# Kernel tuning notes

Measured on AMD Instinct MI355X. Metric: run time of the kernel, lower is better.

Reference implementation:

```python
import jax, jax.numpy as jnp
import numpy as np

N = 2_000_000  # number of Gaussians


def setup_inputs() -> dict:
    key = jax.random.key(0)
    k1, k2, k3 = jax.random.split(key, 3)
    quaternions = jax.random.normal(k1, (N, 4), dtype=jnp.float32)
    scales = jax.random.normal(k2, (N, 3), dtype=jnp.float32) * 0.5
    opacities = jax.random.normal(k3, (N, 1), dtype=jnp.float32)
    return {"quaternions": quaternions, "scales": scales, "opacities": opacities}


def quaternion_to_rotation_matrix(q):
    # q: [N,4] with layout (w, x, y, z) as in the torch source
    w, x, y, z = q[:, 0], q[:, 1], q[:, 2], q[:, 3]
    xx, yy, zz = x * x, y * y, z * z
    xy, xz, yz = x * y, x * z, y * z
    xw, yw, zw = x * w, y * w, z * w
    r0 = jnp.stack([1 - 2 * (yy + zz), 2 * (xy - zw), 2 * (xz + yw)], axis=-1)
    r1 = jnp.stack([2 * (xy + zw), 1 - 2 * (xx + zz), 2 * (yz - xw)], axis=-1)
    r2 = jnp.stack([2 * (xz - yw), 2 * (yz + xw), 1 - 2 * (xx + yy)], axis=-1)
    return jnp.stack([r0, r1, r2], axis=-2)  # [N,3,3]


def reference(quaternions, scales, opacities):
    # sigmoid applied to raw opacities (source: 1/(1+exp(-o)))
    opac = jax.nn.sigmoid(opacities)
    # NOTE: source normalizes by the GLOBAL Frobenius norm of the whole tensor
    # (to.linalg.norm with no dim) -- replicated faithfully.
    qn = quaternions / jnp.linalg.norm(quaternions)
    R = quaternion_to_rotation_matrix(qn)  # [N,3,3]
    # scales_d = (diag(exp(s)))**2 ; scales_i_d = (diag(1/exp(s)))**2
    s2 = jnp.exp(2.0 * scales)      # [N,3] diagonal of S^2
    inv_s2 = jnp.exp(-2.0 * scales)  # [N,3] diagonal of S^-2
    # cov = R @ diag(s2) @ R^T, inv_cov = R @ diag(inv_s2) @ R^T (closed form,
    # no batched 3x3 matmul chain / LAPACK inverse needed)
    cov = jnp.einsum('nij,nj,nkj->nik', R, s2, R)
    inv_cov = jnp.einsum('nij,nj,nkj->nik', R, inv_s2, R)
    return cov, inv_cov, opac
```

## Files before the change

kernel.cpp:

```cpp
#include <hip/hip_runtime.h>
#include <math.h>

#define RBLOCKS 1024
#define RTHREADS 256
#define CHUNK 256
#define BLOCK 256

typedef float f32x4 __attribute__((ext_vector_type(4)));

__global__ __launch_bounds__(RTHREADS) void gp_reduce_sq(
    const float4* __restrict__ q4, int n4, double* __restrict__ partials) {
    __shared__ double sdata[RTHREADS];
    double acc = 0.0;
    int stride = gridDim.x * blockDim.x;
    for (int i = blockIdx.x * blockDim.x + threadIdx.x; i < n4; i += stride) {
        float4 v = q4[i];
        acc += (double)v.x * v.x + (double)v.y * v.y +
               (double)v.z * v.z + (double)v.w * v.w;
    }
    sdata[threadIdx.x] = acc;
    __syncthreads();
    for (int s = RTHREADS / 2; s > 0; s >>= 1) {
        if (threadIdx.x < s) sdata[threadIdx.x] += sdata[threadIdx.x + s];
        __syncthreads();
    }
    if (threadIdx.x == 0) partials[blockIdx.x] = sdata[0];
}

__global__ __launch_bounds__(BLOCK) void gp_main(
    const float4* __restrict__ q,
    const float* __restrict__ scales,
    const float* __restrict__ opac_in,
    const double* __restrict__ partials,
    float* __restrict__ cov,
    float* __restrict__ inv_cov,
    float* __restrict__ opac_out,
    int n) {
    __shared__ union SU {
        double red[4];
        float mat[2 * CHUNK * 9];
    } u;
    __shared__ float s_sc[CHUNK * 3];

    const int tid = threadIdx.x;
    const int c0 = blockIdx.x * CHUNK;
    const int count = min(CHUNK, n - c0);

    float4 qi = make_float4(0.f, 0.f, 0.f, 0.f);
    float op = 0.f;
    if (tid < count) {
        qi = q[c0 + tid];
        op = opac_in[c0 + tid];
    }
    const int nsf = count * 3;
    const int nsf4 = nsf >> 2;
    const float4* sc4 = (const float4*)(scales + (size_t)c0 * 3);
    float4 sv = make_float4(0.f, 0.f, 0.f, 0.f);
    if (tid < nsf4) sv = sc4[tid];

    double acc = 0.0;
#pragma unroll
    for (int k = 0; k < RBLOCKS / 256; ++k) acc += partials[tid + 256 * k];
#pragma unroll
    for (int off = 32; off > 0; off >>= 1) acc += __shfl_down(acc, off);
    if ((tid & 63) == 0) u.red[tid >> 6] = acc;

    if (tid < nsf4) {
        s_sc[4 * tid + 0] = sv.x;
        s_sc[4 * tid + 1] = sv.y;
        s_sc[4 * tid + 2] = sv.z;
        s_sc[4 * tid + 3] = sv.w;
    }
    {
        int r = nsf - (nsf4 << 2);
        if (tid < r) s_sc[(nsf4 << 2) + tid] =
            scales[(size_t)c0 * 3 + (nsf4 << 2) + tid];
    }
    __syncthreads();

    double tot = u.red[0] + u.red[1] + u.red[2] + u.red[3];
    const float inv_norm = (float)(1.0 / sqrt(tot));
    __syncthreads();

    if (tid < count) {
        float w = qi.x * inv_norm;
        float x = qi.y * inv_norm;
        float y = qi.z * inv_norm;
        float z = qi.w * inv_norm;

        float xx = x * x, yy = y * y, zz = z * z;
        float xy = x * y, xz = x * z, yz = y * z;
        float xw = x * w, yw = y * w, zw = z * w;

        float r00 = 1.f - 2.f * (yy + zz);
        float r01 = 2.f * (xy - zw);
        float r02 = 2.f * (xz + yw);
        float r10 = 2.f * (xy + zw);
        float r11 = 1.f - 2.f * (xx + zz);
        float r12 = 2.f * (yz - xw);
        float r20 = 2.f * (xz - yw);
        float r21 = 2.f * (yz + xw);
        float r22 = 1.f - 2.f * (xx + yy);

        float s0 = s_sc[3 * tid + 0];
        float s1 = s_sc[3 * tid + 1];
        float s2 = s_sc[3 * tid + 2];

        float e0 = __expf(2.f * s0), e1 = __expf(2.f * s1), e2 = __expf(2.f * s2);
        float f0 = 1.f / e0, f1 = 1.f / e1, f2 = 1.f / e2;

        float* mc = &u.mat[tid * 9];
        float* mi = &u.mat[CHUNK * 9 + tid * 9];
        {
            float a0 = r00 * e0, a1 = r01 * e1, a2 = r02 * e2;
            float b0 = r10 * e0, b1 = r11 * e1, b2 = r12 * e2;
            float g0 = r20 * e0, g1 = r21 * e1, g2 = r22 * e2;
            float m00 = a0 * r00 + a1 * r01 + a2 * r02;
            float m01 = a0 * r10 + a1 * r11 + a2 * r12;
            float m02 = a0 * r20 + a1 * r21 + a2 * r22;
            float m11 = b0 * r10 + b1 * r11 + b2 * r12;
            float m12 = b0 * r20 + b1 * r21 + b2 * r22;
            float m22 = g0 * r20 + g1 * r21 + g2 * r22;
            mc[0] = m00; mc[1] = m01; mc[2] = m02;
            mc[3] = m01; mc[4] = m11; mc[5] = m12;
            mc[6] = m02; mc[7] = m12; mc[8] = m22;
        }
        {
            float a0 = r00 * f0, a1 = r01 * f1, a2 = r02 * f2;
            float b0 = r10 * f0, b1 = r11 * f1, b2 = r12 * f2;
            float g0 = r20 * f0, g1 = r21 * f1, g2 = r22 * f2;
            float m00 = a0 * r00 + a1 * r01 + a2 * r02;
            float m01 = a0 * r10 + a1 * r11 + a2 * r12;
            float m02 = a0 * r20 + a1 * r21 + a2 * r22;
            float m11 = b0 * r10 + b1 * r11 + b2 * r12;
            float m12 = b0 * r20 + b1 * r21 + b2 * r22;
            float m22 = g0 * r20 + g1 * r21 + g2 * r22;
            mi[0] = m00; mi[1] = m01; mi[2] = m02;
            mi[3] = m01; mi[4] = m11; mi[5] = m12;
            mi[6] = m02; mi[7] = m12; mi[8] = m22;
        }
        opac_out[c0 + tid] = 1.f / (1.f + __expf(-op));
    }
    __syncthreads();

    const int nf = count * 9;
    const int nfv = nf >> 2;
    f32x4* covo = (f32x4*)(cov + (size_t)c0 * 9);
    f32x4* invo = (f32x4*)(inv_cov + (size_t)c0 * 9);
    const f32x4* mc4 = (const f32x4*)u.mat;
    const f32x4* mi4 = (const f32x4*)(u.mat + CHUNK * 9);
    for (int j = tid; j < nfv; j += BLOCK) {
        __builtin_nontemporal_store(mc4[j], covo + j);
        __builtin_nontemporal_store(mi4[j], invo + j);
    }
    for (int j = (nfv << 2) + tid; j < nf; j += BLOCK) {
        cov[(size_t)c0 * 9 + j] = u.mat[j];
        inv_cov[(size_t)c0 * 9 + j] = u.mat[CHUNK * 9 + j];
    }
}

extern "C" void kernel_launch(void* const* d_in, const int* in_sizes, int n_in,
                              void* d_out, int out_size, void* d_ws, size_t ws_size,
                              hipStream_t stream) {
    const float4* q = (const float4*)d_in[0];
    const float* scales = (const float*)d_in[1];
    const float* opac = (const float*)d_in[2];
    int n = in_sizes[0] / 4;

    float* out = (float*)d_out;
    float* cov = out;
    float* inv_cov = out + (size_t)n * 9;
    float* opac_out = out + (size_t)n * 18;

    double* partials = (double*)d_ws;

    gp_reduce_sq<<<RBLOCKS, RTHREADS, 0, stream>>>(q, n, partials);

    int nblocks = (n + CHUNK - 1) / CHUNK;
    gp_main<<<nblocks, BLOCK, 0, stream>>>(
        q, scales, opac, partials, cov, inv_cov, opac_out, n);
}
```

Baseline: 43.61 us.

## Process two chunks per block in main kernel, amortizing partial reduction

Each block of the main kernel now handles two 256-element chunks instead of one, halving the grid. All global loads for both chunks are issued up front, and the reduction of the 1024 double partials to the global norm is done once for both. Chunk B's scales are staged into shared memory right after chunk A's stores are issued, and the opacity output now uses a nontemporal store. The cost is fewer blocks for latency hiding, more live registers, and an extra shared-memory reuse step with more barriers.

Result: slower. 45.23 us (+3.7%).

```diff
diff --git a/kernel.cpp b/kernel.cpp
--- a/kernel.cpp
+++ b/kernel.cpp
@@ -2,15 +2,14 @@
 #include <math.h>
 
 #define RBLOCKS 1024
-#define RTHREADS 256
+#define BLOCK 256
 #define CHUNK 256
-#define BLOCK 256
 
 typedef float f32x4 __attribute__((ext_vector_type(4)));
 
-__global__ __launch_bounds__(RTHREADS) void gp_reduce_sq(
+__global__ __launch_bounds__(BLOCK) void gp_reduce_sq(
     const float4* __restrict__ q4, int n4, double* __restrict__ partials) {
-    __shared__ double sdata[RTHREADS];
+    __shared__ double sdata[BLOCK];
     double acc = 0.0;
     int stride = gridDim.x * blockDim.x;
     for (int i = blockIdx.x * blockDim.x + threadIdx.x; i < n4; i += stride) {
@@ -20,11 +19,102 @@
     }
     sdata[threadIdx.x] = acc;
     __syncthreads();
-    for (int s = RTHREADS / 2; s > 0; s >>= 1) {
+    for (int s = BLOCK / 2; s > 0; s >>= 1) {
         if (threadIdx.x < s) sdata[threadIdx.x] += sdata[threadIdx.x + s];
         __syncthreads();
     }
     if (threadIdx.x == 0) partials[blockIdx.x] = sdata[0];
+}
+
+__device__ __forceinline__ void gp_compute_one(
+    int tid, float4 qi, float s0, float s1, float s2, float inv_norm,
+    float* __restrict__ s_mat) {
+    float w = qi.x * inv_norm;
+    float x = qi.y * inv_norm;
+    float y = qi.z * inv_norm;
+    float z = qi.w * inv_norm;
+
+    float xx = x * x, yy = y * y, zz = z * z;
+    float xy = x * y, xz = x * z, yz = y * z;
+    float xw = x * w, yw = y * w, zw = z * w;
+
+    float r00 = 1.f - 2.f * (yy + zz);
+    float r01 = 2.f * (xy - zw);
+    float r02 = 2.f * (xz + yw);
+    float r10 = 2.f * (xy + zw);
+    float r11 = 1.f - 2.f * (xx + zz);
+    float r12 = 2.f * (yz - xw);
+    float r20 = 2.f * (xz - yw);
+    float r21 = 2.f * (yz + xw);
+    float r22 = 1.f - 2.f * (xx + yy);
+
+    float e0 = __expf(2.f * s0), e1 = __expf(2.f * s1), e2 = __expf(2.f * s2);
+    float f0 = 1.f / e0, f1 = 1.f / e1, f2 = 1.f / e2;
+
+    float* mc = &s_mat[tid * 9];
+    float* mi = &s_mat[CHUNK * 9 + tid * 9];
+    {
+        float a0 = r00 * e0, a1 = r01 * e1, a2 = r02 * e2;
+        float b0 = r10 * e0, b1 = r11 * e1, b2 = r12 * e2;
+        float g0 = r20 * e0, g1 = r21 * e1, g2 = r22 * e2;
+        float m00 = a0 * r00 + a1 * r01 + a2 * r02;
+        float m01 = a0 * r10 + a1 * r11 + a2 * r12;
+        float m02 = a0 * r20 + a1 * r21 + a2 * r22;
+        float m11 = b0 * r10 + b1 * r11 + b2 * r12;
+        float m12 = b0 * r20 + b1 * r21 + b2 * r22;
+        float m22 = g0 * r20 + g1 * r21 + g2 * r22;
+        mc[0] = m00; mc[1] = m01; mc[2] = m02;
+        mc[3] = m01; mc[4] = m11; mc[5] = m12;
+        mc[6] = m02; mc[7] = m12; mc[8] = m22;
+    }
+    {
+        float a0 = r00 * f0, a1 = r01 * f1, a2 = r02 * f2;
+        float b0 = r10 * f0, b1 = r11 * f1, b2 = r12 * f2;
+        float g0 = r20 * f0, g1 = r21 * f1, g2 = r22 * f2;
+        float m00 = a0 * r00 + a1 * r01 + a2 * r02;
+        float m01 = a0 * r10 + a1 * r11 + a2 * r12;
+        float m02 = a0 * r20 + a1 * r21 + a2 * r22;
+        float m11 = b0 * r10 + b1 * r11 + b2 * r12;
+        float m12 = b0 * r20 + b1 * r21 + b2 * r22;
+        float m22 = g0 * r20 + g1 * r21 + g2 * r22;
+        mi[0] = m00; mi[1] = m01; mi[2] = m02;
+        mi[3] = m01; mi[4] = m11; mi[5] = m12;
+        mi[6] = m02; mi[7] = m12; mi[8] = m22;
+    }
+}
+
+__device__ __forceinline__ void gp_stage_scales(
+    int tid, int count, float4 sv, const float* __restrict__ scales,
+    size_t g0, float* __restrict__ s_sc) {
+    const int nsf = count * 3;
+    const int nsf4 = nsf >> 2;
+    if (tid < nsf4) {
+        s_sc[4 * tid + 0] = sv.x;
+        s_sc[4 * tid + 1] = sv.y;
+        s_sc[4 * tid + 2] = sv.z;
+        s_sc[4 * tid + 3] = sv.w;
+    }
+    int r = nsf - (nsf4 << 2);
+    if (tid < r) s_sc[(nsf4 << 2) + tid] = scales[g0 * 3 + (nsf4 << 2) + tid];
+}
+
+__device__ __forceinline__ void gp_store_chunk(
+    int tid, int count, size_t g0, const float* __restrict__ s_mat,
+    float* __restrict__ cov, float* __restrict__ inv_cov) {
+    const int nf = count * 9;
+    const int nfv = nf >> 2;
+    f32x4* covo = (f32x4*)(cov + g0 * 9);
+    f32x4* invo = (f32x4*)(inv_cov + g0 * 9);
+    const f32x4* mc4 = (const f32x4*)s_mat;
+    const f32x4* mi4 = (const f32x4*)(s_mat + CHUNK * 9);
+    for (int j = tid; j < nfv; j += BLOCK) {
+        __builtin_nontemporal_store(mc4[j], covo + j);
+        __builtin_nontemporal_store(mi4[j], invo + j);
+    }
+    for (int j = (nfv << 2) + tid; j < nf; j += BLOCK) {
+        cov[g0 * 9 + j] = s_mat[j];
+        inv_cov[g0 * 9 + j] = s_mat[CHUNK * 9 + j];
+    }
 }
 
 __global__ __launch_bounds__(BLOCK) void gp_main(
@@ -43,20 +133,30 @@
     __shared__ float s_sc[CHUNK * 3];
 
     const int tid = threadIdx.x;
-    const int c0 = blockIdx.x * CHUNK;
-    const int count = min(CHUNK, n - c0);
-
-    float4 qi = make_float4(0.f, 0.f, 0.f, 0.f);
-    float op = 0.f;
-    if (tid < count) {
-        qi = q[c0 + tid];
-        op = opac_in[c0 + tid];
-    }
-    const int nsf = count * 3;
-    const int nsf4 = nsf >> 2;
-    const float4* sc4 = (const float4*)(scales + (size_t)c0 * 3);
-    float4 sv = make_float4(0.f, 0.f, 0.f, 0.f);
-    if (tid < nsf4) sv = sc4[tid];
+    const size_t cA0 = (size_t)blockIdx.x * (2 * CHUNK);
+    const size_t cB0 = cA0 + CHUNK;
+    const int countA = (int)min((long long)CHUNK, (long long)n - (long long)cA0);
+    const int countB = (int)max(0LL,
+        min((long long)CHUNK, (long long)n - (long long)cB0));
+
+    float4 qA = make_float4(0.f, 0.f, 0.f, 0.f);
+    float opA = 0.f;
+    if (tid < countA) {
+        qA = q[cA0 + tid];
+        opA = opac_in[cA0 + tid];
+    }
+    float4 qB = make_float4(0.f, 0.f, 0.f, 0.f);
+    float opB = 0.f;
+    if (tid < countB) {
+        qB = q[cB0 + tid];
+        opB = opac_in[cB0 + tid];
+    }
+    const float4* scA4 = (const float4*)(scales + cA0 * 3);
+    const float4* scB4 = (const float4*)(scales + cB0 * 3);
+    float4 svA = make_float4(0.f, 0.f, 0.f, 0.f);
+    float4 svB = make_float4(0.f, 0.f, 0.f, 0.f);
+    if (tid < (countA * 3) >> 2) svA = scA4[tid];
+    if (tid < (countB * 3) >> 2) svB = scB4[tid];
 
     double acc = 0.0;
 #pragma unroll
@@ -65,98 +165,34 @@
     for (int off = 32; off > 0; off >>= 1) acc += __shfl_down(acc, off);
     if ((tid & 63) == 0) u.red[tid >> 6] = acc;
 
-    if (tid < nsf4) {
-        s_sc[4 * tid + 0] = sv.x;
-        s_sc[4 * tid + 1] = sv.y;
-        s_sc[4 * tid + 2] = sv.z;
-        s_sc[4 * tid + 3] = sv.w;
-    }
-    {
-        int r = nsf - (nsf4 << 2);
-        if (tid < r) s_sc[(nsf4 << 2) + tid] =
-            scales[(size_t)c0 * 3 + (nsf4 << 2) + tid];
-    }
-    __syncthreads();
-
-    double tot = u.red[0] + u.red[1] + u.red[2] + u.red[3];
+    gp_stage_scales(tid, countA, svA, scales, cA0, s_sc);
+    __syncthreads();
+
+    const double tot = u.red[0] + u.red[1] + u.red[2] + u.red[3];
     const float inv_norm = (float)(1.0 / sqrt(tot));
     __syncthreads();
 
-    if (tid < count) {
-        float w = qi.x * inv_norm;
-        float x = qi.y * inv_norm;
-        float y = qi.z * inv_norm;
-        float z = qi.w * inv_norm;
-
-        float xx = x * x, yy = y * y, zz = z * z;
-        float xy = x * y, xz = x * z, yz = y * z;
-        float xw = x * w, yw = y * w, zw = z * w;
-
-        float r00 = 1.f - 2.f * (yy + zz);
-        float r01 = 2.f * (xy - zw);
-        float r02 = 2.f * (xz + yw);
-        float r10 = 2.f * (xy + zw);
-        float r11 = 1.f - 2.f * (xx + zz);
-        float r12 = 2.f * (yz - xw);
-        float r20 = 2.f * (xz - yw);
-        float r21 = 2.f * (yz + xw);
-        float r22 = 1.f - 2.f * (xx + yy);
-
-        float s0 = s_sc[3 * tid + 0];
-        float s1 = s_sc[3 * tid + 1];
-        float s2 = s_sc[3 * tid + 2];
-
-        float e0 = __expf(2.f * s0), e1 = __expf(2.f * s1), e2 = __expf(2.f * s2);
-        float f0 = 1.f / e0, f1 = 1.f / e1, f2 = 1.f / e2;
-
-        float* mc = &u.mat[tid * 9];
-        float* mi = &u.mat[CHUNK * 9 + tid * 9];
-        {
-            float a0 = r00 * e0, a1 = r01 * e1, a2 = r02 * e2;
-            float b0 = r10 * e0, b1 = r11 * e1, b2 = r12 * e2;
-            float g0 = r20 * e0, g1 = r21 * e1, g2 = r22 * e2;
-            float m00 = a0 * r00 + a1 * r01 + a2 * r02;
-            float m01 = a0 * r10 + a1 * r11 + a2 * r12;
-            float m02 = a0 * r20 + a1 * r21 + a2 * r22;
-            float m11 = b0 * r10 + b1 * r11 + b2 * r12;
-            float m12 = b0 * r20 + b1 * r21 + b2 * r22;
-            float m22 = g0 * r20 + g1 * r21 + g2 * r22;
-            mc[0] = m00; mc[1] = m01; mc[2] = m02;
-            mc[3] = m01; mc[4] = m11; mc[5] = m12;
-            mc[6] = m02; mc[7] = m12; mc[8] = m22;
-        }
-        {
-            float a0 = r00 * f0, a1 = r01 * f1, a2 = r02 * f2;
-            float b0 = r10 * f0, b1 = r11 * f1, b2 = r12 * f2;
-            float g0 = r20 * f0, g1 = r21 * f1, g2 = r22 * f2;
-            float m00 = a0 * r00 + a1 * r01 + a2 * r02;
-            float m01 = a0 * r10 + a1 * r11 + a2 * r12;
-            float m02 = a0 * r20 + a1 * r21 + a2 * r22;
-            float m11 = b0 * r10 + b1 * r11 + b2 * r12;
-            float m12 = b0 * r20 + b1 * r21 + b2 * r22;
-            float m22 = g0 * r20 + g1 * r21 + g2 * r22;
-            mi[0] = m00; mi[1] = m01; mi[2] = m02;
-            mi[3] = m01; mi[4] = m11; mi[5] = m12;
-            mi[6] = m02; mi[7] = m12; mi[8] = m22;
-        }
-        opac_out[c0 + tid] = 1.f / (1.f + __expf(-op));
-    }
-    __syncthreads();
-
-    const int nf = count * 9;
-    const int nfv = nf >> 2;
-    f32x4* covo = (f32x4*)(cov + (size_t)c0 * 9);
-    f32x4* invo = (f32x4*)(inv_cov + (size_t)c0 * 9);
-    const f32x4* mc4 = (const f32x4*)u.mat;
-    const f32x4* mi4 = (const f32x4*)(u.mat + CHUNK * 9);
-    for (int j = tid; j < nfv; j += BLOCK) {
-        __builtin_nontemporal_store(mc4[j], covo + j);
-        __builtin_nontemporal_store(mi4[j], invo + j);
-    }
-    for (int j = (nfv << 2) + tid; j < nf; j += BLOCK) {
-        cov[(size_t)c0 * 9 + j] = u.mat[j];
-        inv_cov[(size_t)c0 * 9 + j] = u.mat[CHUNK * 9 + j];
-    }
+    if (tid < countA) {
+        gp_compute_one(tid, qA, s_sc[3 * tid + 0], s_sc[3 * tid + 1],
+                       s_sc[3 * tid + 2], inv_norm, u.mat);
+        __builtin_nontemporal_store(1.f / (1.f + __expf(-opA)),
+                                    opac_out + cA0 + tid);
+    }
+    __syncthreads();
+
+    gp_store_chunk(tid, countA, cA0, u.mat, cov, inv_cov);
+    gp_stage_scales(tid, countB, svB, scales, cB0, s_sc);
+    __syncthreads();
+
+    if (tid < countB) {
+        gp_compute_one(tid, qB, s_sc[3 * tid + 0], s_sc[3 * tid + 1],
+                       s_sc[3 * tid + 2], inv_norm, u.mat);
+        __builtin_nontemporal_store(1.f / (1.f + __expf(-opB)),
+                                    opac_out + cB0 + tid);
+    }
+    __syncthreads();
+
+    gp_store_chunk(tid, countB, cB0, u.mat, cov, inv_cov);
 }
 
 extern "C" void kernel_launch(void* const* d_in, const int* in_sizes, int n_in,
@@ -174,9 +210,9 @@
 
     double* partials = (double*)d_ws;
 
-    gp_reduce_sq<<<RBLOCKS, RTHREADS, 0, stream>>>(q, n, partials);
-
-    int nblocks = (n + CHUNK - 1) / CHUNK;
+    gp_reduce_sq<<<RBLOCKS, BLOCK, 0, stream>>>(q, n, partials);
+
+    int nblocks = (n + 2 * CHUNK - 1) / (2 * CHUNK);
     gp_main<<<nblocks, BLOCK, 0, stream>>>(
         q, scales, opac, partials, cov, inv_cov, opac_out, n);
 }
```
